# Kernel optimization log

Measured on AMD Instinct MI355X. Metric: run time of the kernel, lower is better.

The kernel has to match this reference:

```python
import jax, jax.numpy as jnp
import numpy as np

B = 8192          # batch size
OBS = 128         # observation dim
HID = 512         # input_size / hidden_size
HEADS = 4         # num_input_heads
VSZ = 256         # input_value_size
NU = 64           # num_units (rim_num)
K = 8             # top-k
NOPT = 16         # option_num


def setup_inputs() -> dict:
    key = jax.random.key(0)
    ks = jax.random.split(key, 8)
    return {
        "x": jax.random.normal(ks[0], (B, OBS), dtype=jnp.float32),
        "option": jax.random.randint(ks[1], (B,), 0, NOPT),
        "pre_fc_w": jax.random.normal(ks[2], (OBS, HID), dtype=jnp.float32) * (OBS ** -0.5),
        "pre_fc_b": jax.random.normal(ks[3], (HID,), dtype=jnp.float32) * 0.01,
        "value_w": jax.random.normal(ks[4], (HID, HEADS * VSZ), dtype=jnp.float32) * (HID ** -0.5),
        "value_b": jax.random.normal(ks[5], (HEADS * VSZ,), dtype=jnp.float32) * 0.01,
        "p_w": jax.random.normal(ks[6], (NOPT, NU), dtype=jnp.float32),
        "p_b": jax.random.normal(ks[7], (NU,), dtype=jnp.float32),
    }


def reference(x, option, pre_fc_w, pre_fc_b, value_w, value_b, p_w, p_b):
    b = x.shape[0]
    # pre_fc: [B, OBS] -> [B, HID]
    h = x @ pre_fc_w + pre_fc_b
    # concat null input slot -> [B, 2, HID]
    h2 = jnp.stack([h, jnp.zeros_like(h)], axis=1)
    # one-hot option + null slot -> [B, 2, NOPT]
    oh = jax.nn.one_hot(option, NOPT, dtype=jnp.float32)
    oh2 = jnp.stack([oh, jnp.zeros_like(oh)], axis=1)
    # value projection, split heads, mean over heads -> [B, 2, VSZ]
    v = (h2 @ value_w + value_b).reshape(b, 2, HEADS, VSZ)
    value_layer = jnp.mean(v, axis=2)
    # attention scores: einsum('bio,on->bni') -> [B, NU, 2]
    scores = jnp.einsum('bio,on->bni', oh2, p_w)
    # bias: p_b for real slot, zeros for null slot
    pb = jnp.stack([jnp.broadcast_to(p_b, (b, NU)), jnp.zeros((b, NU), jnp.float32)], axis=2)
    scores = scores + pb
    # top-k unit mask over not-null scores [B, NU]
    not_null = scores[:, :, 0]
    _, topk_idx = jax.lax.top_k(not_null, K)  # [B, K]
    mask = jnp.zeros((b, NU), jnp.float32).at[jnp.arange(b)[:, None], topk_idx].set(1.0)
    # softmax over the 2 slots (dropout is identity at eval)
    probs = jax.nn.softmax(scores, axis=-1)  # [B, NU, 2]
    # attention readout, masked, mean over units -> [B, VSZ]
    inputs = jnp.einsum('bns,bsv->bnv', probs, value_layer) * mask[:, :, None]
    return jnp.mean(inputs, axis=1)
```

## Files before the change

kernel.cpp:

```cpp
#include <hip/hip_runtime.h>
#include <hip/hip_bf16.h>

#define B_N   8192
#define OBS   128
#define HID   512
#define HEADS 4
#define VSZ   256
#define NU    64
#define TOPK  8
#define NOPT  16

typedef __bf16 bf16_t;
typedef __bf16 bf16x8 __attribute__((ext_vector_type(8)));
typedef float  f32x4  __attribute__((ext_vector_type(4)));

#define OFF_WEFF 0u
#define OFF_C    524288u
#define OFF_D    525312u
#define OFF_A    541696u
#define OFF_MT   544768u
#define OFF_XB   610304u

__global__ void k_weff(const float* __restrict__ vw, float* __restrict__ weff) {
    int j = blockIdx.x, v = threadIdx.x;
    const float* r = vw + j * (HEADS * VSZ);
    weff[j * VSZ + v] = 0.25f * (r[v] + r[v + VSZ] + r[v + 2 * VSZ] + r[v + 3 * VSZ]);
}

__global__ void k_m(const float* __restrict__ pw, const float* __restrict__ pb,
                    const float* __restrict__ weff, bf16_t* __restrict__ mt,
                    float* __restrict__ c) {
    int k = blockIdx.x, v = threadIdx.x;
    const float* wr = (k < OBS) ? (pw + k * HID) : pb;
    float a0 = 0.f, a1 = 0.f, a2 = 0.f, a3 = 0.f;
    #pragma unroll 4
    for (int j = 0; j < HID; j += 4) {
        a0 += wr[j + 0] * weff[(j + 0) * VSZ + v];
        a1 += wr[j + 1] * weff[(j + 1) * VSZ + v];
        a2 += wr[j + 2] * weff[(j + 2) * VSZ + v];
        a3 += wr[j + 3] * weff[(j + 3) * VSZ + v];
    }
    float acc = (a0 + a1) + (a2 + a3);
    if (k < OBS) mt[v * OBS + k] = (bf16_t)acc;
    else         c[v] = acc;
}

__global__ void k_coef(const float* __restrict__ p_w, const float* __restrict__ p_b,
                       const float* __restrict__ vb, const float* __restrict__ c,
                       float* __restrict__ A, float* __restrict__ D) {
    __shared__ float sA[NOPT];
    int tid  = threadIdx.x;
    int lane = tid & 63;
    int opt  = tid >> 6;

    float cur = p_w[opt * NU + lane] + p_b[lane];
    float sum = 0.f;
    #pragma unroll
    for (int t = 0; t < TOPK; ++t) {
        float m = cur;
        #pragma unroll
        for (int off = 32; off >= 1; off >>= 1)
            m = fmaxf(m, __shfl_xor(m, off));
        sum += 1.f / (1.f + expf(-m));
        unsigned long long b = __ballot(cur == m);
        int first = __ffsll(b) - 1;
        if (lane == first) cur = -1e30f;
    }
    if (lane == 0) { sA[opt] = sum * (1.f / NU); A[opt] = sA[opt]; }
    __syncthreads();

    if (tid < VSZ) {
        int v = tid;
        float be = 0.25f * (vb[v] + vb[v + VSZ] + vb[v + 2 * VSZ] + vb[v + 3 * VSZ]);
        float cv = c[v];
        #pragma unroll
        for (int o = 0; o < NOPT; ++o)
            D[o * VSZ + v] = sA[o] * cv + 0.125f * be;
    }
}

__global__ void k_cast(const float* __restrict__ x, bf16_t* __restrict__ xb) {
    int i = (blockIdx.x * 256 + threadIdx.x) * 8;
    f32x4 a = *(const f32x4*)(x + i);
    f32x4 b = *(const f32x4*)(x + i + 4);
    bf16x8 o;
    o[0] = (bf16_t)a[0]; o[1] = (bf16_t)a[1]; o[2] = (bf16_t)a[2]; o[3] = (bf16_t)a[3];
    o[4] = (bf16_t)b[0]; o[5] = (bf16_t)b[1]; o[6] = (bf16_t)b[2]; o[7] = (bf16_t)b[3];
    *(bf16x8*)(xb + i) = o;
}

__launch_bounds__(256)
__global__ void k_main(const bf16_t* __restrict__ xb, const bf16_t* __restrict__ mt,
                       const int* __restrict__ opt, const float* __restrict__ A,
                       const float* __restrict__ D, float* __restrict__ out) {
    int wave = threadIdx.x >> 6;
    int lane = threadIdx.x & 63;
    int r0   = blockIdx.x * 64 + wave * 16;
    int c0   = blockIdx.y * 64;
    int mrow = lane & 15;
    int quad = lane >> 4;

    f32x4 acc0 = {0.f, 0.f, 0.f, 0.f};
    f32x4 acc1 = {0.f, 0.f, 0.f, 0.f};
    f32x4 acc2 = {0.f, 0.f, 0.f, 0.f};
    f32x4 acc3 = {0.f, 0.f, 0.f, 0.f};

    const bf16_t* xa = xb + (r0 + mrow) * OBS + quad * 8;
    const bf16_t* mb = mt + (c0 + mrow) * OBS + quad * 8;

    #pragma unroll
    for (int kt = 0; kt < 4; ++kt) {
        bf16x8 a  = *(const bf16x8*)(xa + kt * 32);
        bf16x8 b0 = *(const bf16x8*)(mb + kt * 32);
        bf16x8 b1 = *(const bf16x8*)(mb + 16 * OBS + kt * 32);
        bf16x8 b2 = *(const bf16x8*)(mb + 32 * OBS + kt * 32);
        bf16x8 b3 = *(const bf16x8*)(mb + 48 * OBS + kt * 32);
        acc0 = __builtin_amdgcn_mfma_f32_16x16x32_bf16(a, b0, acc0, 0, 0, 0);
        acc1 = __builtin_amdgcn_mfma_f32_16x16x32_bf16(a, b1, acc1, 0, 0, 0);
        acc2 = __builtin_amdgcn_mfma_f32_16x16x32_bf16(a, b2, acc2, 0, 0, 0);
        acc3 = __builtin_amdgcn_mfma_f32_16x16x32_bf16(a, b3, acc3, 0, 0, 0);
    }

    int col = c0 + mrow;
    #pragma unroll
    for (int r = 0; r < 4; ++r) {
        int row = r0 + quad * 4 + r;
        int o = opt[row];
        float a = A[o];
        const float* Dr = D + o * VSZ;
        out[row * VSZ + col +  0] = a * acc0[r] + Dr[col +  0];
        out[row * VSZ + col + 16] = a * acc1[r] + Dr[col + 16];
        out[row * VSZ + col + 32] = a * acc2[r] + Dr[col + 32];
        out[row * VSZ + col + 48] = a * acc3[r] + Dr[col + 48];
    }
}

extern "C" void kernel_launch(void* const* d_in, const int* in_sizes, int n_in,
                              void* d_out, int out_size, void* d_ws, size_t ws_size,
                              hipStream_t stream) {
    const float* x        = (const float*)d_in[0];
    const int*   option   = (const int*)  d_in[1];
    const float* pre_fc_w = (const float*)d_in[2];
    const float* pre_fc_b = (const float*)d_in[3];
    const float* value_w  = (const float*)d_in[4];
    const float* value_b  = (const float*)d_in[5];
    const float* p_w      = (const float*)d_in[6];
    const float* p_b      = (const float*)d_in[7];
    float* out = (float*)d_out;

    char* ws = (char*)d_ws;
    float*  weff = (float*) (ws + OFF_WEFF);
    float*  c    = (float*) (ws + OFF_C);
    float*  D    = (float*) (ws + OFF_D);
    float*  A    = (float*) (ws + OFF_A);
    bf16_t* mt   = (bf16_t*)(ws + OFF_MT);
    bf16_t* xbuf = (bf16_t*)(ws + OFF_XB);

    k_weff<<<dim3(HID), dim3(VSZ), 0, stream>>>(value_w, weff);
    k_m   <<<dim3(OBS + 1), dim3(VSZ), 0, stream>>>(pre_fc_w, pre_fc_b, weff, mt, c);
    k_coef<<<dim3(1), dim3(NOPT * 64), 0, stream>>>(p_w, p_b, value_b, c, A, D);
    k_cast<<<dim3(B_N * OBS / (256 * 8)), dim3(256), 0, stream>>>(x, xbuf);
    k_main<<<dim3(B_N / 64, VSZ / 64), dim3(256), 0, stream>>>(xbuf, mt, option, A, D, out);
}
```

Measured before the change: 99.66 us.

## Fuse prep kernels, fold bias into an extra K tile, cast x inside main GEMM

Merges the weff and top-k coefficient kernels into one launch and removes the separate x-to-bf16 cast kernel by converting fp32 x in registers inside the MFMA kernel. The c bias row is folded into the M matrix as an extra K column (padded to 160) and multiplied by a constant-one A column, so the per-option D table disappears. The M-construction kernel splits the 512-long reduction across four thread groups with a shared-memory sum, and the main kernel widens its column tile to 128. This cuts launches and the bf16 round trip of x, at the cost of an extra MFMA K step, fp32 x loads in the hot kernel and bf16 rounding of the bias term.

Result: faster. 97.60 us (-2.1%).

```diff
diff --git a/kernel.cpp b/kernel.cpp
--- a/kernel.cpp
+++ b/kernel.cpp
@@ -9,129 +9,131 @@
 #define NU    64
 #define TOPK  8
 #define NOPT  16
+#define KEXT  160
 
 typedef __bf16 bf16_t;
 typedef __bf16 bf16x8 __attribute__((ext_vector_type(8)));
 typedef float  f32x4  __attribute__((ext_vector_type(4)));
 
 #define OFF_WEFF 0u
-#define OFF_C    524288u
-#define OFF_D    525312u
-#define OFF_A    541696u
-#define OFF_MT   544768u
-#define OFF_XB   610304u
+#define OFF_A    524288u
+#define OFF_DP   524352u
+#define OFF_MT   525376u
 
-__global__ void k_weff(const float* __restrict__ vw, float* __restrict__ weff) {
-    int j = blockIdx.x, v = threadIdx.x;
-    const float* r = vw + j * (HEADS * VSZ);
-    weff[j * VSZ + v] = 0.25f * (r[v] + r[v + VSZ] + r[v + 2 * VSZ] + r[v + 3 * VSZ]);
+__global__ void k_pre(const float* __restrict__ vw, const float* __restrict__ p_w,
+                      const float* __restrict__ p_b, const float* __restrict__ vb,
+                      float* __restrict__ weff, float* __restrict__ A,
+                      float* __restrict__ Dp) {
+    if (blockIdx.x < HID) {
+        int j = blockIdx.x, v = threadIdx.x;
+        const float* r = vw + j * (HEADS * VSZ);
+        weff[j * VSZ + v] = 0.25f * (r[v] + r[v + VSZ] + r[v + 2 * VSZ] + r[v + 3 * VSZ]);
+        return;
+    }
+    int tid  = threadIdx.x;
+    int lane = tid & 63;
+    int w    = tid >> 6;
+    #pragma unroll
+    for (int oo = 0; oo < 4; ++oo) {
+        int o = w * 4 + oo;
+        float cur = p_w[o * NU + lane] + p_b[lane];
+        float sum = 0.f;
+        #pragma unroll
+        for (int t = 0; t < TOPK; ++t) {
+            float m = cur;
+            #pragma unroll
+            for (int off = 32; off >= 1; off >>= 1)
+                m = fmaxf(m, __shfl_xor(m, off));
+            sum += 1.f / (1.f + expf(-m));
+            unsigned long long bal = __ballot(cur == m);
+            int first = __ffsll(bal) - 1;
+            if (lane == first) cur = -1e30f;
+        }
+        if (lane == 0) A[o] = sum * (1.f / NU);
+    }
+    if (tid < VSZ)
+        Dp[tid] = 0.125f * 0.25f * (vb[tid] + vb[tid + VSZ] + vb[tid + 2 * VSZ] + vb[tid + 3 * VSZ]);
 }
 
-__global__ void k_m(const float* __restrict__ pw, const float* __restrict__ pb,
-                    const float* __restrict__ weff, bf16_t* __restrict__ mt,
-                    float* __restrict__ c) {
-    int k = blockIdx.x, v = threadIdx.x;
+__global__ void k_mt(const float* __restrict__ pw, const float* __restrict__ pb,
+                     const float* __restrict__ weff, bf16_t* __restrict__ mt) {
+    int k  = blockIdx.x;
+    int v  = threadIdx.x & 255;
+    int jq = threadIdx.x >> 8;
+    __shared__ float red[1024];
+    if (k > 128) {
+        if (threadIdx.x < VSZ) mt[v * KEXT + k] = (bf16_t)0.f;
+        return;
+    }
     const float* wr = (k < OBS) ? (pw + k * HID) : pb;
+    const float* wj = wr + jq * 128;
+    const float* wf = weff + (jq * 128) * VSZ + v;
     float a0 = 0.f, a1 = 0.f, a2 = 0.f, a3 = 0.f;
     #pragma unroll 4
-    for (int j = 0; j < HID; j += 4) {
-        a0 += wr[j + 0] * weff[(j + 0) * VSZ + v];
-        a1 += wr[j + 1] * weff[(j + 1) * VSZ + v];
-        a2 += wr[j + 2] * weff[(j + 2) * VSZ + v];
-        a3 += wr[j + 3] * weff[(j + 3) * VSZ + v];
+    for (int j = 0; j < 128; j += 4) {
+        a0 += wj[j + 0] * wf[(j + 0) * VSZ];
+        a1 += wj[j + 1] * wf[(j + 1) * VSZ];
+        a2 += wj[j + 2] * wf[(j + 2) * VSZ];
+        a3 += wj[j + 3] * wf[(j + 3) * VSZ];
     }
-    float acc = (a0 + a1) + (a2 + a3);
-    if (k < OBS) mt[v * OBS + k] = (bf16_t)acc;
-    else         c[v] = acc;
-}
-
-__global__ void k_coef(const float* __restrict__ p_w, const float* __restrict__ p_b,
-                       const float* __restrict__ vb, const float* __restrict__ c,
-                       float* __restrict__ A, float* __restrict__ D) {
-    __shared__ float sA[NOPT];
-    int tid  = threadIdx.x;
-    int lane = tid & 63;
-    int opt  = tid >> 6;
-
-    float cur = p_w[opt * NU + lane] + p_b[lane];
-    float sum = 0.f;
-    #pragma unroll
-    for (int t = 0; t < TOPK; ++t) {
-        float m = cur;
-        #pragma unroll
-        for (int off = 32; off >= 1; off >>= 1)
-            m = fmaxf(m, __shfl_xor(m, off));
-        sum += 1.f / (1.f + expf(-m));
-        unsigned long long b = __ballot(cur == m);
-        int first = __ffsll(b) - 1;
-        if (lane == first) cur = -1e30f;
-    }
-    if (lane == 0) { sA[opt] = sum * (1.f / NU); A[opt] = sA[opt]; }
+    red[threadIdx.x] = (a0 + a1) + (a2 + a3);
     __syncthreads();
-
-    if (tid < VSZ) {
-        int v = tid;
-        float be = 0.25f * (vb[v] + vb[v + VSZ] + vb[v + 2 * VSZ] + vb[v + 3 * VSZ]);
-        float cv = c[v];
-        #pragma unroll
-        for (int o = 0; o < NOPT; ++o)
-            D[o * VSZ + v] = sA[o] * cv + 0.125f * be;
+    if (jq == 0) {
+        float s = red[v] + red[v + 256] + red[v + 512] + red[v + 768];
+        mt[v * KEXT + k] = (bf16_t)s;
     }
 }
 
-__global__ void k_cast(const float* __restrict__ x, bf16_t* __restrict__ xb) {
-    int i = (blockIdx.x * 256 + threadIdx.x) * 8;
-    f32x4 a = *(const f32x4*)(x + i);
-    f32x4 b = *(const f32x4*)(x + i + 4);
-    bf16x8 o;
-    o[0] = (bf16_t)a[0]; o[1] = (bf16_t)a[1]; o[2] = (bf16_t)a[2]; o[3] = (bf16_t)a[3];
-    o[4] = (bf16_t)b[0]; o[5] = (bf16_t)b[1]; o[6] = (bf16_t)b[2]; o[7] = (bf16_t)b[3];
-    *(bf16x8*)(xb + i) = o;
-}
-
 __launch_bounds__(256)
-__global__ void k_main(const bf16_t* __restrict__ xb, const bf16_t* __restrict__ mt,
+__global__ void k_main(const float* __restrict__ x, const bf16_t* __restrict__ mt,
                        const int* __restrict__ opt, const float* __restrict__ A,
-                       const float* __restrict__ D, float* __restrict__ out) {
+                       const float* __restrict__ Dp, float* __restrict__ out) {
     int wave = threadIdx.x >> 6;
     int lane = threadIdx.x & 63;
-    int r0   = blockIdx.x * 64 + wave * 16;
-    int c0   = blockIdx.y * 64;
     int mrow = lane & 15;
     int quad = lane >> 4;
+    int r0   = blockIdx.x * 64 + wave * 16;
+    int c0   = blockIdx.y * 128;
 
-    f32x4 acc0 = {0.f, 0.f, 0.f, 0.f};
-    f32x4 acc1 = {0.f, 0.f, 0.f, 0.f};
-    f32x4 acc2 = {0.f, 0.f, 0.f, 0.f};
-    f32x4 acc3 = {0.f, 0.f, 0.f, 0.f};
+    f32x4 acc[8];
+    #pragma unroll
+    for (int t = 0; t < 8; ++t) acc[t] = (f32x4){0.f, 0.f, 0.f, 0.f};
 
-    const bf16_t* xa = xb + (r0 + mrow) * OBS + quad * 8;
-    const bf16_t* mb = mt + (c0 + mrow) * OBS + quad * 8;
+    const float*  xr = x + (r0 + mrow) * OBS + quad * 8;
+    const bf16_t* mb = mt + (c0 + mrow) * KEXT + quad * 8;
 
     #pragma unroll
-    for (int kt = 0; kt < 4; ++kt) {
-        bf16x8 a  = *(const bf16x8*)(xa + kt * 32);
-        bf16x8 b0 = *(const bf16x8*)(mb + kt * 32);
-        bf16x8 b1 = *(const bf16x8*)(mb + 16 * OBS + kt * 32);
-        bf16x8 b2 = *(const bf16x8*)(mb + 32 * OBS + kt * 32);
-        bf16x8 b3 = *(const bf16x8*)(mb + 48 * OBS + kt * 32);
-        acc0 = __builtin_amdgcn_mfma_f32_16x16x32_bf16(a, b0, acc0, 0, 0, 0);
-        acc1 = __builtin_amdgcn_mfma_f32_16x16x32_bf16(a, b1, acc1, 0, 0, 0);
-        acc2 = __builtin_amdgcn_mfma_f32_16x16x32_bf16(a, b2, acc2, 0, 0, 0);
-        acc3 = __builtin_amdgcn_mfma_f32_16x16x32_bf16(a, b3, acc3, 0, 0, 0);
+    for (int kt = 0; kt < 5; ++kt) {
+        bf16x8 a;
+        if (kt < 4) {
+            f32x4 lo = *(const f32x4*)(xr + kt * 32);
+            f32x4 hi = *(const f32x4*)(xr + kt * 32 + 4);
+            a[0] = (bf16_t)lo[0]; a[1] = (bf16_t)lo[1];
+            a[2] = (bf16_t)lo[2]; a[3] = (bf16_t)lo[3];
+            a[4] = (bf16_t)hi[0]; a[5] = (bf16_t)hi[1];
+            a[6] = (bf16_t)hi[2]; a[7] = (bf16_t)hi[3];
+        } else {
+            #pragma unroll
+            for (int j = 0; j < 8; ++j) a[j] = (bf16_t)0.f;
+            if (quad == 0) a[0] = (bf16_t)1.0f;
+        }
+        #pragma unroll
+        for (int t = 0; t < 8; ++t) {
+            bf16x8 b = *(const bf16x8*)(mb + t * 16 * KEXT + kt * 32);
+            acc[t] = __builtin_amdgcn_mfma_f32_16x16x32_bf16(a, b, acc[t], 0, 0, 0);
+        }
     }
 
-    int col = c0 + mrow;
     #pragma unroll
     for (int r = 0; r < 4; ++r) {
         int row = r0 + quad * 4 + r;
-        int o = opt[row];
-        float a = A[o];
-        const float* Dr = D + o * VSZ;
-        out[row * VSZ + col +  0] = a * acc0[r] + Dr[col +  0];
-        out[row * VSZ + col + 16] = a * acc1[r] + Dr[col + 16];
-        out[row * VSZ + col + 32] = a * acc2[r] + Dr[col + 32];
-        out[row * VSZ + col + 48] = a * acc3[r] + Dr[col + 48];
+        float av = A[opt[row]];
+        float* orow = out + row * VSZ;
+        #pragma unroll
+        for (int t = 0; t < 8; ++t) {
+            int col = c0 + t * 16 + mrow;
+            orow[col] = av * acc[t][r] + Dp[col];
+        }
     }
 }
 
@@ -150,15 +152,11 @@
 
     char* ws = (char*)d_ws;
     float*  weff = (float*) (ws + OFF_WEFF);
-    float*  c    = (float*) (ws + OFF_C);
-    float*  D    = (float*) (ws + OFF_D);
     float*  A    = (float*) (ws + OFF_A);
+    float*  Dp   = (float*) (ws + OFF_DP);
     bf16_t* mt   = (bf16_t*)(ws + OFF_MT);
-    bf16_t* xbuf = (bf16_t*)(ws + OFF_XB);
 
-    k_weff<<<dim3(HID), dim3(VSZ), 0, stream>>>(value_w, weff);
-    k_m   <<<dim3(OBS + 1), dim3(VSZ), 0, stream>>>(pre_fc_w, pre_fc_b, weff, mt, c);
-    k_coef<<<dim3(1), dim3(NOPT * 64), 0, stream>>>(p_w, p_b, value_b, c, A, D);
-    k_cast<<<dim3(B_N * OBS / (256 * 8)), dim3(256), 0, stream>>>(x, xbuf);
-    k_main<<<dim3(B_N / 64, VSZ / 64), dim3(256), 0, stream>>>(xbuf, mt, option, A, D, out);
+    k_pre <<<dim3(HID + 1), dim3(VSZ), 0, stream>>>(value_w, p_w, p_b, value_b, weff, A, Dp);
+    k_mt  <<<dim3(KEXT), dim3(1024), 0, stream>>>(pre_fc_w, pre_fc_b, weff, mt);
+    k_main<<<dim3(B_N / 64, VSZ / 128), dim3(256), 0, stream>>>(x, mt, option, A, Dp, out);
 }
```
